# Kernel tuning notes

Hardware: AMD Instinct MI355X
Metric: run time of the kernel (lower is better)

## Reference

```python
import jax, jax.numpy as jnp
import numpy as np

B, N, D_MODEL, H = 4, 2048, 1024, 16  # batch, seq, model dim, heads


def setup_inputs() -> dict:
    key = jax.random.key(0)
    k1, k2, k3 = jax.random.split(key, 3)
    x = jax.random.normal(k1, (B, N, D_MODEL), dtype=jnp.float32)
    # nn.Linear weights: [out_features, in_features]; scaled for stability
    Wqkv = jax.random.normal(k2, (3 * D_MODEL, D_MODEL), dtype=jnp.float32) * 0.02
    bqkv = jnp.zeros((3 * D_MODEL,), dtype=jnp.float32)
    Wo = jax.random.normal(k3, (D_MODEL, D_MODEL), dtype=jnp.float32) * 0.02
    bo = jnp.zeros((D_MODEL,), dtype=jnp.float32)
    return {"x": x, "Wqkv": Wqkv, "bqkv": bqkv, "Wo": Wo, "bo": bo}


def reference(x, Wqkv, bqkv, Wo, bo):
    b, n, _ = x.shape
    qkv = x @ Wqkv.T + bqkv                      # [b, n, 3*d_model]
    # rearrange 'b n (h d) -> b h n d' with h heads, then chunk into q,k,v
    qkv = qkv.reshape(b, n, H, -1).transpose(0, 2, 1, 3)  # [b, h, n, 3*dh]
    q, k, v = jnp.split(qkv, 3, axis=-1)          # each [b, h, n, dh]
    scale = k.shape[-1] ** 0.5
    scores = jnp.einsum('bhqd,bhkd->bhqk', q, k) / scale
    attn = jax.nn.softmax(scores, axis=-1)
    out = jnp.einsum('bhqk,bhkd->bhqd', attn, v)  # [b, h, n, dh]
    out = out.transpose(0, 2, 1, 3).reshape(b, n, -1)  # 'b h n d -> b n (h d)'
    return out @ Wo.T + bo
```

## Files before the change

kernel.cpp:

```cpp
#include <hip/hip_runtime.h>
#include <hip/hip_bf16.h>

using bf16 = __hip_bfloat16;
typedef __attribute__((ext_vector_type(8))) __bf16 bf16x8;
typedef __attribute__((ext_vector_type(4))) float f32x4;
typedef __attribute__((ext_vector_type(16))) float f32x16;
typedef __attribute__((ext_vector_type(4))) unsigned u32x4;

#define MFMA16(a, b, c) __builtin_amdgcn_mfma_f32_16x16x32_bf16((a), (b), (c), 0, 0, 0)
#define MFMA32(a, b, c) __builtin_amdgcn_mfma_f32_32x32x16_bf16((a), (b), (c), 0, 0, 0)

static __device__ __forceinline__ void gload_lds16(const bf16* g, bf16* l) {
    __builtin_amdgcn_global_load_lds(
        (__attribute__((address_space(1))) void*)(bf16*)(g),
        (__attribute__((address_space(3))) void*)(l), 16, 0, 0);
}

static __device__ __forceinline__ unsigned cvtpk(float lo, float hi) {
    unsigned r;
    asm("v_cvt_pk_bf16_f32 %0, %1, %2" : "=v"(r) : "v"(lo), "v"(hi));
    return r;
}

__global__ void cvt_all(const float* __restrict__ x, const float* __restrict__ wq,
                        const float* __restrict__ wo,
                        bf16* __restrict__ xb, bf16* __restrict__ wqb, bf16* __restrict__ wob) {
    int b = blockIdx.x;
    const float* src;
    bf16* dst;
    long i;
    if (b < 8192)       { src = x;  dst = xb;  i = (long)b * 256 + threadIdx.x; }
    else if (b < 11264) { src = wq; dst = wqb; i = (long)(b - 8192) * 256 + threadIdx.x; }
    else                { src = wo; dst = wob; i = (long)(b - 11264) * 256 + threadIdx.x; }
    float4 v = ((const float4*)src)[i];
    bf16 t[4];
    t[0] = __float2bfloat16(v.x);
    t[1] = __float2bfloat16(v.y);
    t[2] = __float2bfloat16(v.z);
    t[3] = __float2bfloat16(v.w);
    *(uint2*)(dst + 4l * i) = *(uint2*)t;
}

__global__ void gemm_qkv(const bf16* __restrict__ A, const bf16* __restrict__ B,
                         const float* __restrict__ bias,
                         bf16* __restrict__ Qo, bf16* __restrict__ Ko, bf16* __restrict__ Vt) {
    const int K = 1024;
    __shared__ bf16 Alds[2][4096];
    __shared__ bf16 Blds[2][4096];
    int t = threadIdx.x;
    int lane = t & 63;
    int wave = t >> 6;
    int wm = wave >> 1, wn = wave & 1;
    int r = lane & 15, q = lane >> 4;
    int lin = blockIdx.x;
    int xcd = lin & 7, rr_ = lin >> 3;
    int mi = xcd * 8 + rr_ / 24;
    int ni = rr_ % 24;
    long m0 = (long)mi * 128;
    long n0 = (long)ni * 128;
    const bf16* Ab = A + m0 * K;
    const bf16* Bb = B + n0 * K;

    f32x4 acc[4][4] = {};

    int srow = t >> 2;
    int scol = (t & 3) << 3;

    auto stage = [&](int buf, int k0) {
        gload_lds16(Ab + (long)srow * K + k0 + scol, Alds[buf] + t * 8);
        gload_lds16(Ab + (long)(srow + 64) * K + k0 + scol, Alds[buf] + 2048 + t * 8);
        gload_lds16(Bb + (long)srow * K + k0 + scol, Blds[buf] + t * 8);
        gload_lds16(Bb + (long)(srow + 64) * K + k0 + scol, Blds[buf] + 2048 + t * 8);
    };
    auto compute = [&](int buf) {
        bf16x8 af[4], bfv[4];
#pragma unroll
        for (int mi4 = 0; mi4 < 4; mi4++)
            af[mi4] = *(const bf16x8*)(Alds[buf] + (wm * 64 + mi4 * 16 + r) * 32 + q * 8);
#pragma unroll
        for (int ni4 = 0; ni4 < 4; ni4++)
            bfv[ni4] = *(const bf16x8*)(Blds[buf] + (wn * 64 + ni4 * 16 + r) * 32 + q * 8);
#pragma unroll
        for (int mi4 = 0; mi4 < 4; mi4++)
#pragma unroll
            for (int ni4 = 0; ni4 < 4; ni4++)
                acc[mi4][ni4] = MFMA16(af[mi4], bfv[ni4], acc[mi4][ni4]);
    };

    stage(0, 0);
    __syncthreads();
    int cur = 0;
    for (int k0 = 32; k0 < K; k0 += 32) {
        stage(cur ^ 1, k0);
        compute(cur);
        __syncthreads();
        cur ^= 1;
    }
    compute(cur);

#pragma unroll
    for (int ni4 = 0; ni4 < 4; ni4++) {
        int n = (int)n0 + wn * 64 + ni4 * 16 + r;
        float bn = bias[n];
        int h = n / 192;
        int rem = n % 192;
        int part = rem >> 6;
        int d = rem & 63;
#pragma unroll
        for (int mi4 = 0; mi4 < 4; mi4++) {
#pragma unroll
            for (int rr = 0; rr < 4; rr++) {
                int m = (int)m0 + wm * 64 + mi4 * 16 + q * 4 + rr;
                int b = m >> 11;
                int row = m & 2047;
                long bh = b * 16 + h;
                bf16 bv = __float2bfloat16(acc[mi4][ni4][rr] + bn);
                if (part == 0)      Qo[(bh * 2048 + row) * 64 + d] = bv;
                else if (part == 1) Ko[(bh * 2048 + row) * 64 + d] = bv;
                else                Vt[(bh * 64 + d) * 2048 + row] = bv;
            }
        }
    }
}


#define PACK8(S, OFF, OUTV) { \
    unsigned A0 = cvtpk(S[OFF+0], S[OFF+1]); \
    unsigned B0 = cvtpk(S[OFF+4], S[OFF+5]); \
    unsigned A1 = cvtpk(S[OFF+2], S[OFF+3]); \
    unsigned B1 = cvtpk(S[OFF+6], S[OFF+7]); \
    asm("v_permlane32_swap_b32 %0, %1" : "+v"(A0), "+v"(B0)); \
    asm("v_permlane32_swap_b32 %0, %1" : "+v"(A1), "+v"(B1)); \
    u32x4 W; W.x = A0; W.y = A1; W.z = B0; W.w = B1; \
    OUTV = __builtin_bit_cast(bf16x8, W); }

#define COMPUTE(KB, VB) do { \
    f32x16 sA = {}, sB = {}; \
    __builtin_amdgcn_s_setprio(1); \
    { \
        bf16x8 kA, kB; \
        kA = *(const bf16x8*)(KB + (0 * 64 + lane) * 8); \
        kB = *(const bf16x8*)(KB + (256 + 0 * 64 + lane) * 8); \
        sA = MFMA32(kA, qf0, sA);  sB = MFMA32(kB, qf0, sB); \
        kA = *(const bf16x8*)(KB + (1 * 64 + lane) * 8); \
        kB = *(const bf16x8*)(KB + (256 + 1 * 64 + lane) * 8); \
        sA = MFMA32(kA, qf1, sA);  sB = MFMA32(kB, qf1, sB); \
        kA = *(const bf16x8*)(KB + (2 * 64 + lane) * 8); \
        kB = *(const bf16x8*)(KB + (256 + 2 * 64 + lane) * 8); \
        sA = MFMA32(kA, qf2, sA);  sB = MFMA32(kB, qf2, sB); \
        kA = *(const bf16x8*)(KB + (3 * 64 + lane) * 8); \
        kB = *(const bf16x8*)(KB + (256 + 3 * 64 + lane) * 8); \
        sA = MFMA32(kA, qf3, sA);  sB = MFMA32(kB, qf3, sB); \
    } \
    __builtin_amdgcn_s_setprio(0); \
    float x0 = fmaxf(fmaxf(sA[0], sA[1]), fmaxf(sA[2], sA[3])); \
    float x1 = fmaxf(fmaxf(sA[4], sA[5]), fmaxf(sA[6], sA[7])); \
    float x2 = fmaxf(fmaxf(sA[8], sA[9]), fmaxf(sA[10], sA[11])); \
    float x3 = fmaxf(fmaxf(sA[12], sA[13]), fmaxf(sA[14], sA[15])); \
    float y0 = fmaxf(fmaxf(sB[0], sB[1]), fmaxf(sB[2], sB[3])); \
    float y1 = fmaxf(fmaxf(sB[4], sB[5]), fmaxf(sB[6], sB[7])); \
    float y2 = fmaxf(fmaxf(sB[8], sB[9]), fmaxf(sB[10], sB[11])); \
    float y3 = fmaxf(fmaxf(sB[12], sB[13]), fmaxf(sB[14], sB[15])); \
    float pm = fmaxf(fmaxf(fmaxf(x0, x1), fmaxf(x2, x3)), \
                     fmaxf(fmaxf(y0, y1), fmaxf(y2, y3))); \
    pm = fmaxf(pm, __shfl_xor(pm, 32)); \
    bool resc = !__all(pm <= mv + 8.0f); \
    if (resc) { \
        float mn = fmaxf(mv, pm); \
        float al = __builtin_amdgcn_exp2f((mv - mn) * C1); \
        mv = mn; \
        lv *= al; \
        _Pragma("unroll") for (int e = 0; e < 16; ++e) { o0[e] *= al; o1[e] *= al; } \
    } \
    float mc = mv * C1; \
    _Pragma("unroll") for (int e = 0; e < 16; ++e) sA[e] = __builtin_amdgcn_exp2f(sA[e] * C1 - mc); \
    _Pragma("unroll") for (int e = 0; e < 16; ++e) sB[e] = __builtin_amdgcn_exp2f(sB[e] * C1 - mc); \
    { \
        f32x16 scv = sA + sB; \
        float u0 = (scv[0] + scv[1]) + (scv[2] + scv[3]); \
        float u1 = (scv[4] + scv[5]) + (scv[6] + scv[7]); \
        float u2 = (scv[8] + scv[9]) + (scv[10] + scv[11]); \
        float u3 = (scv[12] + scv[13]) + (scv[14] + scv[15]); \
        float ts = (u0 + u1) + (u2 + u3); \
        ts += __shfl_xor(ts, 32); \
        lv += ts; \
    } \
    bf16x8 pf0, pf1, pf2, pf3; \
    PACK8(sA, 0, pf0); PACK8(sA, 8, pf1); PACK8(sB, 0, pf2); PACK8(sB, 8, pf3); \
    __builtin_amdgcn_s_setprio(1); \
    { \
        bf16x8 vA, vB; \
        vA = *(const bf16x8*)(VB + (0 * 64 + lane) * 8); \
        vB = *(const bf16x8*)(VB + (256 + 0 * 64 + lane) * 8); \
        o0 = MFMA32(vA, pf0, o0);  o1 = MFMA32(vB, pf0, o1); \
        vA = *(const bf16x8*)(VB + (1 * 64 + lane) * 8); \
        vB = *(const bf16x8*)(VB + (256 + 1 * 64 + lane) * 8); \
        o0 = MFMA32(vA, pf1, o0);  o1 = MFMA32(vB, pf1, o1); \
        vA = *(const bf16x8*)(VB + (2 * 64 + lane) * 8); \
        vB = *(const bf16x8*)(VB + (256 + 2 * 64 + lane) * 8); \
        o0 = MFMA32(vA, pf2, o0);  o1 = MFMA32(vB, pf2, o1); \
        vA = *(const bf16x8*)(VB + (3 * 64 + lane) * 8); \
        vB = *(const bf16x8*)(VB + (256 + 3 * 64 + lane) * 8); \
        o0 = MFMA32(vA, pf3, o0);  o1 = MFMA32(vB, pf3, o1); \
    } \
    __builtin_amdgcn_s_setprio(0); \
} while (0)

__global__ __launch_bounds__(512, 4) void attn_fwd(const bf16* __restrict__ Q,
                                                   const bf16* __restrict__ Kg,
                                                   const bf16* __restrict__ Vt,
                                                   bf16* __restrict__ AO) {
    __shared__ bf16 smem[16384];
    bf16* K0 = smem;
    bf16* V0 = smem + 4096;
    bf16* K1 = smem + 8192;
    bf16* V1 = smem + 12288;
    const int t = threadIdx.x;
    const int lane = t & 63, wave = t >> 6;
    const int l31 = lane & 31, hi = lane >> 5;
    const int bid = blockIdx.x;
    const int xcd = bid & 7, idx = bid >> 3;
    const int bh = xcd * 8 + (idx >> 3);
    const int qt = idx & 7;
    const float C1 = 0.18033688011112042f;

    bf16x8 qf0, qf1, qf2, qf3;
    {
        const bf16* Qb = Q + ((long)bh * 2048 + qt * 256 + wave * 32 + l31) * 64 + hi * 8;
        qf0 = *(const bf16x8*)(Qb + 0);
        qf1 = *(const bf16x8*)(Qb + 16);
        qf2 = *(const bf16x8*)(Qb + 32);
        qf3 = *(const bf16x8*)(Qb + 48);
    }

    const bf16* Kh = Kg + (long)bh * 2048 * 64;
    const bf16* Vh = Vt + (long)bh * 64 * 2048;

    const int sr = ((t >> 8) << 5) + (t & 31);
    const int sc = ((t >> 6) & 3) * 16 + ((t >> 5) & 1) * 8;

    f32x16 o0 = {}, o1 = {};
    float mv = -1e30f, lv = 0.f;

    auto issue_stage = [&](bf16* Kb, bf16* Vb, int kv0) {
        gload_lds16(Kh + (long)(kv0 + sr) * 64 + sc, Kb + t * 8);
        gload_lds16(Vh + (long)sr * 2048 + kv0 + sc, Vb + t * 8);
    };

    issue_stage(K0, V0, 0);
    __syncthreads();

    for (int kv0 = 0;; kv0 += 128) {
        issue_stage(K1, V1, kv0 + 64);
        COMPUTE(K0, V0);
        __syncthreads();
        if (kv0 + 128 < 2048) issue_stage(K0, V0, kv0 + 128);
        COMPUTE(K1, V1);
        if (kv0 + 128 >= 2048) break;
        __syncthreads();
    }

    long bb = bh >> 4, hh = bh & 15;
    __syncthreads();
    float il = 1.f / lv;
    char* wbase = (char*)smem + wave * 4096 + l31 * 128;
#pragma unroll
    for (int j = 0; j < 4; ++j) {
        unsigned wlo = cvtpk(o0[4 * j] * il, o0[4 * j + 1] * il);
        unsigned whi = cvtpk(o0[4 * j + 2] * il, o0[4 * j + 3] * il);
        int b8 = 2 * j + hi;
        int b8s = b8 ^ ((l31 & 7) << 1);
        uint2 val; val.x = wlo; val.y = whi;
        *(uint2*)(wbase + b8s * 8) = val;
    }
#pragma unroll
    for (int j = 0; j < 4; ++j) {
        unsigned wlo = cvtpk(o1[4 * j] * il, o1[4 * j + 1] * il);
        unsigned whi = cvtpk(o1[4 * j + 2] * il, o1[4 * j + 3] * il);
        int b8 = 8 + 2 * j + hi;
        int b8s = b8 ^ ((l31 & 7) << 1);
        uint2 val; val.x = wlo; val.y = whi;
        *(uint2*)(wbase + b8s * 8) = val;
    }
    __syncthreads();
    {
        int rid = t >> 1, hf = t & 1;
        int wv = rid >> 5, qq = rid & 31;
        long orow = (long)qt * 256 + wv * 32 + qq;
        const char* rbase = (const char*)smem + wv * 4096 + qq * 128;
        bf16* dst = AO + (bb * 2048 + orow) * 1024 + hh * 64 + hf * 32;
#pragma unroll
        for (int k = 0; k < 4; ++k) {
            int b8 = hf * 8 + 2 * k;
            int b8s = b8 ^ ((qq & 7) << 1);
            int4 v = *(const int4*)(rbase + b8s * 8);
            *(int4*)(dst + k * 8) = v;
        }
    }
}

__global__ void gemm_out(const bf16* __restrict__ A, const bf16* __restrict__ B,
                         const float* __restrict__ bias, float* __restrict__ C) {
    const int K = 1024, N = 1024;
    __shared__ bf16 Alds[2][4096];
    __shared__ bf16 Blds[2][4096];
    int t = threadIdx.x;
    int lane = t & 63;
    int wave = t >> 6;
    int wm = wave >> 1, wn = wave & 1;
    int r = lane & 15, q = lane >> 4;
    int lin = blockIdx.x;
    int xcd = lin & 7, rr_ = lin >> 3;
    int mi = xcd * 8 + (rr_ >> 3);
    int ni = rr_ & 7;
    long m0 = (long)mi * 128;
    long n0 = (long)ni * 128;
    const bf16* Ab = A + m0 * K;
    const bf16* Bb = B + n0 * K;

    f32x4 acc[4][4] = {};

    int srow = t >> 2;
    int scol = (t & 3) << 3;

    auto stage = [&](int buf, int k0) {
        gload_lds16(Ab + (long)srow * K + k0 + scol, Alds[buf] + t * 8);
        gload_lds16(Ab + (long)(srow + 64) * K + k0 + scol, Alds[buf] + 2048 + t * 8);
        gload_lds16(Bb + (long)srow * K + k0 + scol, Blds[buf] + t * 8);
        gload_lds16(Bb + (long)(srow + 64) * K + k0 + scol, Blds[buf] + 2048 + t * 8);
    };
    auto compute = [&](int buf) {
        bf16x8 af[4], bfv[4];
#pragma unroll
        for (int mi4 = 0; mi4 < 4; mi4++)
            af[mi4] = *(const bf16x8*)(Alds[buf] + (wm * 64 + mi4 * 16 + r) * 32 + q * 8);
#pragma unroll
        for (int ni4 = 0; ni4 < 4; ni4++)
            bfv[ni4] = *(const bf16x8*)(Blds[buf] + (wn * 64 + ni4 * 16 + r) * 32 + q * 8);
#pragma unroll
        for (int mi4 = 0; mi4 < 4; mi4++)
#pragma unroll
            for (int ni4 = 0; ni4 < 4; ni4++)
                acc[mi4][ni4] = MFMA16(af[mi4], bfv[ni4], acc[mi4][ni4]);
    };

    stage(0, 0);
    __syncthreads();
    int cur = 0;
    for (int k0 = 32; k0 < K; k0 += 32) {
        stage(cur ^ 1, k0);
        compute(cur);
        __syncthreads();
        cur ^= 1;
    }
    compute(cur);

#pragma unroll
    for (int ni4 = 0; ni4 < 4; ni4++) {
        int n = (int)n0 + wn * 64 + ni4 * 16 + r;
        float bn = bias[n];
#pragma unroll
        for (int mi4 = 0; mi4 < 4; mi4++) {
#pragma unroll
            for (int rr = 0; rr < 4; rr++) {
                long m = m0 + wm * 64 + mi4 * 16 + q * 4 + rr;
                C[m * N + n] = acc[mi4][ni4][rr] + bn;
            }
        }
    }
}

extern "C" void kernel_launch(void* const* d_in, const int* in_sizes, int n_in,
                              void* d_out, int out_size, void* d_ws, size_t ws_size,
                              hipStream_t stream) {
    const float* x    = (const float*)d_in[0];
    const float* Wqkv = (const float*)d_in[1];
    const float* bqkv = (const float*)d_in[2];
    const float* Wo   = (const float*)d_in[3];
    const float* bo   = (const float*)d_in[4];
    float* out = (float*)d_out;

    char* ws = (char*)d_ws;
    bf16* Xb  = (bf16*)(ws + 0);
    bf16* Wqb = (bf16*)(ws + 16777216);
    bf16* Wob = (bf16*)(ws + 23068672);
    bf16* Qb  = (bf16*)(ws + 25165824);
    bf16* Kb  = (bf16*)(ws + 41943040);
    bf16* Vtb = (bf16*)(ws + 58720256);
    bf16* AOb = (bf16*)(ws + 75497472);

    cvt_all<<<12288, 256, 0, stream>>>(x, Wqkv, Wo, Xb, Wqb, Wob);

    gemm_qkv<<<1536, 256, 0, stream>>>(Xb, Wqb, bqkv, Qb, Kb, Vtb);
    attn_fwd<<<512, 512, 0, stream>>>(Qb, Kb, Vtb, AOb);
    gemm_out<<<512, 256, 0, stream>>>(AOb, Wob, bo, out);
}
```

Measured before the change: 201.3 us.

## Use explicit vmcnt waits and raw barriers to keep two stages in flight

```diff
diff --git a/kernel.cpp b/kernel.cpp
--- a/kernel.cpp
+++ b/kernel.cpp
@@ -9,6 +9,13 @@
 
 #define MFMA16(a, b, c) __builtin_amdgcn_mfma_f32_16x16x32_bf16((a), (b), (c), 0, 0, 0)
 #define MFMA32(a, b, c) __builtin_amdgcn_mfma_f32_32x32x16_bf16((a), (b), (c), 0, 0, 0)
+
+#define WAITV4 asm volatile("s_waitcnt vmcnt(4)" ::: "memory")
+#define WAITV2 asm volatile("s_waitcnt vmcnt(2)" ::: "memory")
+#define WAITV0 asm volatile("s_waitcnt vmcnt(0)" ::: "memory")
+#define WAITL0 asm volatile("s_waitcnt lgkmcnt(0)" ::: "memory")
+#define BAR    __builtin_amdgcn_s_barrier()
+#define SCHED0 __builtin_amdgcn_sched_barrier(0)
 
 static __device__ __forceinline__ void gload_lds16(const bf16* g, bf16* l) {
     __builtin_amdgcn_global_load_lds(
@@ -41,12 +48,56 @@
     *(uint2*)(dst + 4l * i) = *(uint2*)t;
 }
 
+
+#define GEMM_STAGE(AB, BB, K0)                                             \
+    do {                                                                   \
+        gload_lds16(Ab + (long)srow * K + (K0) + scol, (AB) + t * 8);      \
+        gload_lds16(Ab + (long)(srow + 64) * K + (K0) + scol, (AB) + 2048 + t * 8); \
+        gload_lds16(Bb + (long)srow * K + (K0) + scol, (BB) + t * 8);      \
+        gload_lds16(Bb + (long)(srow + 64) * K + (K0) + scol, (BB) + 2048 + t * 8); \
+    } while (0)
+
+#define GEMM_COMPUTE(AB, BB)                                               \
+    do {                                                                   \
+        bf16x8 af[4], bfv[4];                                              \
+        _Pragma("unroll") for (int mi4 = 0; mi4 < 4; mi4++)                \
+            af[mi4] = *(const bf16x8*)((AB) + (wm * 64 + mi4 * 16 + r) * 32 + q * 8); \
+        _Pragma("unroll") for (int ni4 = 0; ni4 < 4; ni4++)                \
+            bfv[ni4] = *(const bf16x8*)((BB) + (wn * 64 + ni4 * 16 + r) * 32 + q * 8); \
+        __builtin_amdgcn_s_setprio(1);                                     \
+        _Pragma("unroll") for (int mi4 = 0; mi4 < 4; mi4++)                \
+            _Pragma("unroll") for (int ni4 = 0; ni4 < 4; ni4++)            \
+                acc[mi4][ni4] = MFMA16(af[mi4], bfv[ni4], acc[mi4][ni4]);  \
+        __builtin_amdgcn_s_setprio(0);                                     \
+    } while (0)
+
+#define GEMM_MAIN_LOOP                                                     \
+    GEMM_STAGE(A0, B0, 0);                                                 \
+    GEMM_STAGE(A1, B1, 32);                                                \
+    for (int k0 = 0; k0 < K - 64; k0 += 64) {                              \
+        WAITV4; BAR; SCHED0;                                               \
+        GEMM_COMPUTE(A0, B0);                                              \
+        WAITL0; BAR; SCHED0;                                               \
+        GEMM_STAGE(A0, B0, k0 + 64);                                       \
+        WAITV4; BAR; SCHED0;                                               \
+        GEMM_COMPUTE(A1, B1);                                              \
+        WAITL0; BAR; SCHED0;                                               \
+        if (k0 + 96 < K) GEMM_STAGE(A1, B1, k0 + 96);                      \
+    }                                                                      \
+    WAITV4; BAR; SCHED0;                                                   \
+    GEMM_COMPUTE(A0, B0);                                                  \
+    WAITV0; BAR; SCHED0;                                                   \
+    GEMM_COMPUTE(A1, B1);
+
 __global__ void gemm_qkv(const bf16* __restrict__ A, const bf16* __restrict__ B,
                          const float* __restrict__ bias,
                          bf16* __restrict__ Qo, bf16* __restrict__ Ko, bf16* __restrict__ Vt) {
     const int K = 1024;
-    __shared__ bf16 Alds[2][4096];
-    __shared__ bf16 Blds[2][4096];
+    __shared__ bf16 smem[16384];
+    bf16* A0 = smem;
+    bf16* B0 = smem + 4096;
+    bf16* A1 = smem + 8192;
+    bf16* B1 = smem + 12288;
     int t = threadIdx.x;
     int lane = t & 63;
     int wave = t >> 6;
@@ -66,37 +117,7 @@
     int srow = t >> 2;
     int scol = (t & 3) << 3;
 
-    auto stage = [&](int buf, int k0) {
-        gload_lds16(Ab + (long)srow * K + k0 + scol, Alds[buf] + t * 8);
-        gload_lds16(Ab + (long)(srow + 64) * K + k0 + scol, Alds[buf] + 2048 + t * 8);
-        gload_lds16(Bb + (long)srow * K + k0 + scol, Blds[buf] + t * 8);
-        gload_lds16(Bb + (long)(srow + 64) * K + k0 + scol, Blds[buf] + 2048 + t * 8);
-    };
-    auto compute = [&](int buf) {
-        bf16x8 af[4], bfv[4];
-#pragma unroll
-        for (int mi4 = 0; mi4 < 4; mi4++)
-            af[mi4] = *(const bf16x8*)(Alds[buf] + (wm * 64 + mi4 * 16 + r) * 32 + q * 8);
-#pragma unroll
-        for (int ni4 = 0; ni4 < 4; ni4++)
-            bfv[ni4] = *(const bf16x8*)(Blds[buf] + (wn * 64 + ni4 * 16 + r) * 32 + q * 8);
-#pragma unroll
-        for (int mi4 = 0; mi4 < 4; mi4++)
-#pragma unroll
-            for (int ni4 = 0; ni4 < 4; ni4++)
-                acc[mi4][ni4] = MFMA16(af[mi4], bfv[ni4], acc[mi4][ni4]);
-    };
-
-    stage(0, 0);
-    __syncthreads();
-    int cur = 0;
-    for (int k0 = 32; k0 < K; k0 += 32) {
-        stage(cur ^ 1, k0);
-        compute(cur);
-        __syncthreads();
-        cur ^= 1;
-    }
-    compute(cur);
+    GEMM_MAIN_LOOP
 
 #pragma unroll
     for (int ni4 = 0; ni4 < 4; ni4++) {
@@ -125,13 +146,13 @@
 
 
 #define PACK8(S, OFF, OUTV) { \
-    unsigned A0 = cvtpk(S[OFF+0], S[OFF+1]); \
-    unsigned B0 = cvtpk(S[OFF+4], S[OFF+5]); \
-    unsigned A1 = cvtpk(S[OFF+2], S[OFF+3]); \
-    unsigned B1 = cvtpk(S[OFF+6], S[OFF+7]); \
-    asm("v_permlane32_swap_b32 %0, %1" : "+v"(A0), "+v"(B0)); \
-    asm("v_permlane32_swap_b32 %0, %1" : "+v"(A1), "+v"(B1)); \
-    u32x4 W; W.x = A0; W.y = A1; W.z = B0; W.w = B1; \
+    unsigned A0_ = cvtpk(S[OFF+0], S[OFF+1]); \
+    unsigned B0_ = cvtpk(S[OFF+4], S[OFF+5]); \
+    unsigned A1_ = cvtpk(S[OFF+2], S[OFF+3]); \
+    unsigned B1_ = cvtpk(S[OFF+6], S[OFF+7]); \
+    asm("v_permlane32_swap_b32 %0, %1" : "+v"(A0_), "+v"(B0_)); \
+    asm("v_permlane32_swap_b32 %0, %1" : "+v"(A1_), "+v"(B1_)); \
+    u32x4 W; W.x = A0_; W.y = A1_; W.z = B0_; W.w = B1_; \
     OUTV = __builtin_bit_cast(bf16x8, W); }
 
 #define COMPUTE(KB, VB) do { \
@@ -248,17 +269,22 @@
     };
 
     issue_stage(K0, V0, 0);
-    __syncthreads();
-
-    for (int kv0 = 0;; kv0 += 128) {
-        issue_stage(K1, V1, kv0 + 64);
+    issue_stage(K1, V1, 64);
+
+    for (int kv0 = 0; kv0 < 2048 - 128; kv0 += 128) {
+        WAITV2; BAR; SCHED0;
         COMPUTE(K0, V0);
-        __syncthreads();
-        if (kv0 + 128 < 2048) issue_stage(K0, V0, kv0 + 128);
+        WAITL0; BAR; SCHED0;
+        issue_stage(K0, V0, kv0 + 128);
+        WAITV2; BAR; SCHED0;
         COMPUTE(K1, V1);
-        if (kv0 + 128 >= 2048) break;
-        __syncthreads();
-    }
+        WAITL0; BAR; SCHED0;
+        if (kv0 + 192 < 2048) issue_stage(K1, V1, kv0 + 192);
+    }
+    WAITV2; BAR; SCHED0;
+    COMPUTE(K0, V0);
+    WAITV0; BAR; SCHED0;
+    COMPUTE(K1, V1);
 
     long bb = bh >> 4, hh = bh & 15;
     __syncthreads();
@@ -302,8 +328,11 @@
 __global__ void gemm_out(const bf16* __restrict__ A, const bf16* __restrict__ B,
                          const float* __restrict__ bias, float* __restrict__ C) {
     const int K = 1024, N = 1024;
-    __shared__ bf16 Alds[2][4096];
-    __shared__ bf16 Blds[2][4096];
+    __shared__ bf16 smem[16384];
+    bf16* A0 = smem;
+    bf16* B0 = smem + 4096;
+    bf16* A1 = smem + 8192;
+    bf16* B1 = smem + 12288;
     int t = threadIdx.x;
     int lane = t & 63;
     int wave = t >> 6;
@@ -323,37 +352,7 @@
     int srow = t >> 2;
     int scol = (t & 3) << 3;
 
-    auto stage = [&](int buf, int k0) {
-        gload_lds16(Ab + (long)srow * K + k0 + scol, Alds[buf] + t * 8);
-        gload_lds16(Ab + (long)(srow + 64) * K + k0 + scol, Alds[buf] + 2048 + t * 8);
-        gload_lds16(Bb + (long)srow * K + k0 + scol, Blds[buf] + t * 8);
-        gload_lds16(Bb + (long)(srow + 64) * K + k0 + scol, Blds[buf] + 2048 + t * 8);
-    };
-    auto compute = [&](int buf) {
-        bf16x8 af[4], bfv[4];
-#pragma unroll
-        for (int mi4 = 0; mi4 < 4; mi4++)
-            af[mi4] = *(const bf16x8*)(Alds[buf] + (wm * 64 + mi4 * 16 + r) * 32 + q * 8);
-#pragma unroll
-        for (int ni4 = 0; ni4 < 4; ni4++)
-            bfv[ni4] = *(const bf16x8*)(Blds[buf] + (wn * 64 + ni4 * 16 + r) * 32 + q * 8);
-#pragma unroll
-        for (int mi4 = 0; mi4 < 4; mi4++)
-#pragma unroll
-            for (int ni4 = 0; ni4 < 4; ni4++)
-                acc[mi4][ni4] = MFMA16(af[mi4], bfv[ni4], acc[mi4][ni4]);
-    };
-
-    stage(0, 0);
-    __syncthreads();
-    int cur = 0;
-    for (int k0 = 32; k0 < K; k0 += 32) {
-        stage(cur ^ 1, k0);
-        compute(cur);
-        __syncthreads();
-        cur ^= 1;
-    }
-    compute(cur);
+    GEMM_MAIN_LOOP
 
 #pragma unroll
     for (int ni4 = 0; ni4 < 4; ni4++) {
```

After: 202.0 us. No clear change (+0.3%).
